# Kernel tuning notes

Measured on AMD Instinct MI355X. Metric: run time of the kernel, lower is better.

## Reference

```python
import jax, jax.numpy as jnp
import numpy as np

N_PROT = 100_000; E_PROT = 1_600_000
N_LIG = 5_000;    E_LIG = 80_000
B_PROT = 64; B_LIG = 1
SEQ = 130; D = 45; K = 4; DIN = 74
PROT_DIMS = [DIN, 50, 45, 45]
LIG_DIMS  = [DIN, 50, 45, 45, 45]
HEAD = [SEQ * D, 2000, 1000, 500, 1]


def setup_inputs() -> dict:
    key = jax.random.key(0)
    ks = iter(jax.random.split(key, 64))
    def rn(shape, scale=1.0):
        return jax.random.normal(next(ks), shape, jnp.float32) * scale
    inp = {
        "prot_x": rn((N_PROT, DIN)),
        "lig_x": rn((N_LIG, DIN)),
    }
    for pref, dims in (("prot", PROT_DIMS), ("lig", LIG_DIMS)):
        for i in range(len(dims) - 1):
            fan_in = (K + 1) * dims[i]
            inp[f"{pref}_W{i}"] = rn((fan_in, dims[i + 1]), fan_in ** -0.5)
            inp[f"{pref}_b{i}"] = jnp.zeros((dims[i + 1],), jnp.float32)
    inp["qkv_w"] = rn((D, 3 * D), D ** -0.5)
    inp["qkv_b"] = jnp.zeros((3 * D,), jnp.float32)
    inp["proj_w"] = rn((D, D), D ** -0.5)
    inp["proj_b"] = jnp.zeros((D,), jnp.float32)
    for i in range(3):
        inp[f"h{i}_w"] = rn((HEAD[i], HEAD[i + 1]), HEAD[i] ** -0.5)
        inp[f"h{i}_b"] = jnp.zeros((HEAD[i + 1],), jnp.float32)
    inp["fc_w"] = rn((HEAD[3], HEAD[4]), HEAD[3] ** -0.5)
    inp["fc_b"] = jnp.zeros((HEAD[4],), jnp.float32)
    inp["prot_src"] = jax.random.randint(next(ks), (E_PROT,), 0, N_PROT, jnp.int32)
    inp["prot_dst"] = jax.random.randint(next(ks), (E_PROT,), 0, N_PROT, jnp.int32)
    # deterministic contiguous subgraph ids guarantee all 64 pockets are non-empty
    inp["prot_gid"] = (jnp.arange(N_PROT) * B_PROT // N_PROT).astype(jnp.int32)
    inp["lig_src"] = jax.random.randint(next(ks), (E_LIG,), 0, N_LIG, jnp.int32)
    inp["lig_dst"] = jax.random.randint(next(ks), (E_LIG,), 0, N_LIG, jnp.int32)
    inp["lig_gid"] = jnp.zeros((N_LIG,), jnp.int32)
    inp["training"] = 0
    return inp


def _tagconv(x, src, dst, W, b, n):
    # DGL TAGConv: h_{k+1} = D^{-1/2} A D^{-1/2} h_k ; out = [h_0..h_K] @ W + b
    deg = jax.ops.segment_sum(jnp.ones_like(dst, x.dtype), dst, num_segments=n)
    norm = jnp.where(deg > 0, deg, 1.0) ** -0.5  # clamp(min=1)^-0.5
    hops = [x]
    h = x
    for _ in range(K):
        h = norm[:, None] * jax.ops.segment_sum((h * norm[:, None])[src], dst, num_segments=n)
        hops.append(h)
    return jnp.concatenate(hops, axis=-1) @ W + b


def _l2norm(x):
    # F.normalize(dim=1): x / max(||x||_2, eps)
    return x / jnp.maximum(jnp.linalg.norm(x, axis=1, keepdims=True), 1e-12)


def _gnn(x, src, dst, gid, Ws, bs, n, ngraphs):
    for W, b in zip(Ws, bs):
        x = _l2norm(jax.nn.relu(_tagconv(x, src, dst, W, b, n)))
        # dropout is identity in eval mode
    return jax.ops.segment_max(x, gid, num_segments=ngraphs)  # DGL MaxPooling


def reference(prot_x, lig_x,
              prot_W0, prot_b0, prot_W1, prot_b1, prot_W2, prot_b2,
              lig_W0, lig_b0, lig_W1, lig_b1, lig_W2, lig_b2, lig_W3, lig_b3,
              qkv_w, qkv_b, proj_w, proj_b,
              h0_w, h0_b, h1_w, h1_b, h2_w, h2_b, fc_w, fc_b,
              prot_src, prot_dst, prot_gid, lig_src, lig_dst, lig_gid, training):
    prot_rep = _gnn(prot_x, prot_src, prot_dst, prot_gid,
                    [prot_W0, prot_W1, prot_W2], [prot_b0, prot_b1, prot_b2],
                    N_PROT, B_PROT)                    # [B_PROT, 45]
    lig_rep = _gnn(lig_x, lig_src, lig_dst, lig_gid,
                   [lig_W0, lig_W1, lig_W2, lig_W3], [lig_b0, lig_b1, lig_b2, lig_b3],
                   N_LIG, B_LIG)                       # [B_LIG, 45]
    n_seq = B_LIG + B_PROT
    seq = jnp.concatenate([lig_rep, prot_rep], axis=0)  # [n_seq, 45]
    seq = jnp.pad(seq, ((0, SEQ - n_seq), (0, 0)))[None]  # [1, 130, 45]

    # eye-based mask exactly as the torch code builds it
    idx = jnp.arange(SEQ)
    valid = idx < n_seq
    mask = jnp.eye(SEQ, dtype=jnp.float32) * (valid[:, None] & valid[None, :])
    mask = mask.at[:, n_seq - 1].set(1.0)
    mask = mask.at[n_seq - 1, :].set(1.0)
    mask = mask.at[n_seq - 1, n_seq - 1].set(0.0)

    qkv = seq @ qkv_w + qkv_b                 # [1, 130, 135]
    q, k, v = jnp.split(qkv, 3, axis=-1)      # single head, head_dim = 45
    attn = jnp.einsum("bqd,bkd->bqk", q, k) * (D ** -0.5)
    attn = jnp.where(mask[None] == 0, -1e9, attn)
    attn = jax.nn.softmax(attn, axis=-1)
    out = jnp.einsum("bqk,bkd->bqd", attn, v) @ proj_w + proj_b  # [1,130,45]

    out = out.reshape(1, SEQ * D)             # [1, 5850]
    for w, b in ((h0_w, h0_b), (h1_w, h1_b), (h2_w, h2_b)):
        out = jax.nn.relu(out @ w + b)        # head dropout off in eval
    return jax.nn.sigmoid(out @ fc_w + fc_b)  # [1, 1]
```

## Files before the change

kernel.cpp:

```cpp
#include <hip/hip_runtime.h>
#include <hip/hip_fp16.h>
#include <cstddef>
#include <cstdint>

namespace {

typedef _Float16 h2v __attribute__((ext_vector_type(2)));

constexpr int NPROT = 100000;
constexpr int EPROT = 1600000;
constexpr int NLIG  = 5000;
constexpr int ELIG  = 80000;


__global__ void hist_kernel(const int* __restrict__ dst, int* __restrict__ cnt, int e) {
  int i = blockIdx.x * 256 + threadIdx.x;
  if (i < e) atomicAdd(&cnt[dst[i]], 1);
}

__global__ void scan1_kernel(const int* __restrict__ cnt, int* __restrict__ rp,
                             int* __restrict__ bsum, float* __restrict__ nrm, int n) {
  __shared__ int wsum[4];
  int t = threadIdx.x;
  int base = blockIdx.x * 1024 + t * 4;
  int v0 = 0, v1 = 0, v2 = 0, v3 = 0;
  if (base + 3 < n) {
    int4 val = *(const int4*)(cnt + base);
    v0 = val.x; v1 = val.y; v2 = val.z; v3 = val.w;
  } else if (base < n) {
    v0 = cnt[base];
    if (base + 1 < n) v1 = cnt[base + 1];
    if (base + 2 < n) v2 = cnt[base + 2];
  }
  if (base < n)     nrm[base]     = 1.0f / sqrtf(fmaxf((float)v0, 1.0f));
  if (base + 1 < n) nrm[base + 1] = 1.0f / sqrtf(fmaxf((float)v1, 1.0f));
  if (base + 2 < n) nrm[base + 2] = 1.0f / sqrtf(fmaxf((float)v2, 1.0f));
  if (base + 3 < n) nrm[base + 3] = 1.0f / sqrtf(fmaxf((float)v3, 1.0f));
  int ts = v0 + v1 + v2 + v3;
  int lane = t & 63, wv = t >> 6;
  int incl = ts;
  #pragma unroll
  for (int off = 1; off < 64; off <<= 1) {
    int o = __shfl_up(incl, off, 64);
    if (lane >= off) incl += o;
  }
  if (lane == 63) wsum[wv] = incl;
  __syncthreads();
  int woff = 0;
  #pragma unroll
  for (int i = 0; i < 4; ++i) if (i < wv) woff += wsum[i];
  int excl = woff + incl - ts;
  int o0 = excl, o1 = o0 + v0, o2 = o1 + v1, o3 = o2 + v2;
  if (base + 3 < n) {
    *(int4*)(rp + base) = make_int4(o0, o1, o2, o3);
  } else if (base < n) {
    rp[base] = o0;
    if (base + 1 < n) rp[base + 1] = o1;
    if (base + 2 < n) rp[base + 2] = o2;
  }
  if (t == 255) bsum[blockIdx.x] = woff + incl;
}

__global__ void scan2_kernel(int* __restrict__ bsum, int nb, int* __restrict__ rp_end) {
  __shared__ int s[256];
  int t = threadIdx.x;
  int v = (t < nb) ? bsum[t] : 0;
  s[t] = v;
  __syncthreads();
  int val = v;
  for (int off = 1; off < 256; off <<= 1) {
    int add = (t >= off) ? s[t - off] : 0;
    __syncthreads();
    val += add;
    s[t] = val;
    __syncthreads();
  }
  if (t < nb) bsum[t] = val - v;
  if (t == 255) *rp_end = val;
}

__global__ void scan3_kernel(int* __restrict__ rp, const int* __restrict__ bsum, int n) {
  int i = blockIdx.x * 256 + threadIdx.x;
  if (i < n) rp[i] += bsum[i >> 10];
}


__global__ void gcur_init_kernel(const int* __restrict__ rp, int* __restrict__ gcur, int n) {
  int t = threadIdx.x;
  if (t < 64) gcur[t] = rp[min(t << 11, n)];
}

__global__ void scat1_kernel(const int* __restrict__ src, const int* __restrict__ dst,
                             int* __restrict__ gcur, uint2* __restrict__ ebuf, int e) {
  __shared__ int lh[64], lb[64];
  int t = threadIdx.x;
  if (t < 64) lh[t] = 0;
  __syncthreads();
  int base = blockIdx.x * 4096;
  int d[16], rk[16];
  #pragma unroll
  for (int j = 0; j < 16; ++j) {
    int i = base + j * 256 + t;
    if (i < e) {
      d[j] = dst[i];
      rk[j] = atomicAdd(&lh[min(d[j] >> 11, 63)], 1);
    }
  }
  __syncthreads();
  if (t < 64 && lh[t] > 0) lb[t] = atomicAdd(&gcur[t], lh[t]);
  __syncthreads();
  #pragma unroll
  for (int j = 0; j < 16; ++j) {
    int i = base + j * 256 + t;
    if (i < e)
      ebuf[lb[min(d[j] >> 11, 63)] + rk[j]] = make_uint2((unsigned)src[i], (unsigned)d[j]);
  }
}

__global__ void scat2_kernel(const uint2* __restrict__ ebuf, const int* __restrict__ rp,
                             int* __restrict__ cur, int* __restrict__ col, int e) {
  int i = blockIdx.x * 256 + threadIdx.x;
  if (i < e) {
    uint2 p = ebuf[i];
    int d = (int)p.y;
    int q = rp[d] + atomicAdd(&cur[d], 1);
    col[q] = (int)p.x;
  }
}


__device__ __forceinline__ float2 cvt_h2(uint32_t u) {
  __half2 h = *reinterpret_cast<__half2*>(&u);
  return make_float2(__low2float(h), __high2float(h));
}

__device__ __forceinline__ h2v bit_h2v(uint32_t u) {
  h2v r;
  *reinterpret_cast<uint32_t*>(&r) = u;
  return r;
}

__global__ void gather_all_kernel(const __half* __restrict__ gin, const int* __restrict__ rp,
                                  const int* __restrict__ col, const float* __restrict__ nrm,
                                  __half* __restrict__ gout, int n, int nbn) {
  int pass = blockIdx.x / nbn;
  int bid = blockIdx.x - pass * nbn;
  int lane = threadIdx.x & 63, wv = threadIdx.x >> 6;
  int q = lane >> 4, r = lane & 15;
  int e_slot = r >> 2, f4 = r & 3;
  int v = bid * 16 + wv * 4 + q;
  bool vok = (v < n);
  int beg = 0, deg = 0;
  if (vok) { beg = rp[v]; deg = rp[v + 1] - beg; }
  const __half* gc = gin + (size_t)pass * n * 16;
  __half* go = gout + (size_t)pass * n * 16;
  float a0 = 0.f, a1 = 0.f, a2 = 0.f, a3 = 0.f;
  for (int base = 0; __any(base < deg); base += 16) {
    int ec = (base + r < deg) ? col[beg + base + r] : -1;
    #pragma unroll
    for (int js = 0; js < 16; js += 4) {
      int sl = (q << 4) + js + e_slot;
      int s0 = __shfl(ec, sl, 64);
      int idx = (s0 >= 0) ? s0 : 0;
      float m = (s0 >= 0) ? 1.f : 0.f;
      uint2 u = *(const uint2*)(gc + (size_t)idx * 16 + (f4 << 2));
      float2 p0 = cvt_h2(u.x), p1 = cvt_h2(u.y);
      a0 = fmaf(m, p0.x, a0); a1 = fmaf(m, p0.y, a1);
      a2 = fmaf(m, p1.x, a2); a3 = fmaf(m, p1.y, a3);
    }
  }
  a0 += __shfl_xor(a0, 4, 64);  a1 += __shfl_xor(a1, 4, 64);
  a2 += __shfl_xor(a2, 4, 64);  a3 += __shfl_xor(a3, 4, 64);
  a0 += __shfl_xor(a0, 8, 64);  a1 += __shfl_xor(a1, 8, 64);
  a2 += __shfl_xor(a2, 8, 64);  a3 += __shfl_xor(a3, 8, 64);
  if (vok && e_slot == 0) {
    float nm = nrm[v];
    float nm2 = nm * nm;
    __half2 w0 = __floats2half2_rn(a0 * nm2, a1 * nm2);
    __half2 w1 = __floats2half2_rn(a2 * nm2, a3 * nm2);
    uint2 st;
    st.x = *reinterpret_cast<uint32_t*>(&w0);
    st.y = *reinterpret_cast<uint32_t*>(&w1);
    *(uint2*)(go + ((size_t)v << 4) + (f4 << 2)) = st;
  }
}

template<int DIN>
__global__ void init_g0_kernel(const float* __restrict__ x, const float* __restrict__ nrm,
                               __half* __restrict__ g0, int n) {
  constexpr int PD = (DIN + 15) & ~15;
  int lane = threadIdx.x & 63;
  int v = blockIdx.x * 4 + (threadIdx.x >> 6);
  if (v >= n) return;
  float nm = nrm[v];
  for (int f = lane; f < PD; f += 64) {
    float val = (f < DIN) ? x[(size_t)v * DIN + f] * nm : 0.f;
    g0[(((size_t)(f >> 4) * n + v) << 4) + (f & 15)] = __float2half(val);
  }
}

__global__ void padw2_kernel(const float* __restrict__ W, uint32_t* __restrict__ Wt,
                             int din, int dout, int pd) {
  int kp2 = 5 * pd / 2;
  int total = dout * kp2;
  int i = blockIdx.x * 256 + threadIdx.x;
  if (i >= total) return;
  int j = i / kp2, k2 = i - j * kp2;
  int f0 = k2 * 2, f1 = f0 + 1;
  int hop0 = f0 / pd, rem0 = f0 - hop0 * pd;
  int hop1 = f1 / pd, rem1 = f1 - hop1 * pd;
  float a = (rem0 < din) ? W[(size_t)(hop0 * din + rem0) * dout + j] : 0.f;
  float b = (rem1 < din) ? W[(size_t)(hop1 * din + rem1) * dout + j] : 0.f;
  __half2 h = __floats2half2_rn(a, b);
  Wt[i] = *reinterpret_cast<uint32_t*>(&h);
}

template<int DIN, int DOUT, bool LAST>
__global__ __launch_bounds__(256) void combine_kernel(
    const __half* __restrict__ gbase, const float* __restrict__ nrm,
    const uint32_t* __restrict__ Wt, const float* __restrict__ bias,
    __half* __restrict__ gnext, float* __restrict__ Xout, int n) {
  constexpr int PD  = (DIN + 15) & ~15;
  constexpr int NCH = PD / 16;
  constexpr int KP2 = 5 * PD / 2;
  constexpr int PDN = (DOUT + 15) & ~15;
  constexpr int QO  = ((DOUT + 7) / 8) * 2;
  __shared__ float ssq[4 * 64];
  int lane = threadIdx.x & 63, wv = threadIdx.x >> 6;
  int v = blockIdx.x * 64 + lane;
  bool vok = (v < n);
  int vc = vok ? v : 0;
  const size_t slabh = (size_t)n * 80;
  int cofs = __builtin_amdgcn_readfirstlane(wv) * QO;
  float acc[QO];
  #pragma unroll
  for (int jj = 0; jj < QO; ++jj) acc[jj] = 0.f;
  for (int hop = 0; hop < 5; ++hop) {
    const __half* hrow = gbase + (size_t)hop * slabh + ((size_t)vc << 4);
    #pragma unroll 1
    for (int ch = 0; ch < NCH; ++ch) {
      uint4 u0 = *(const uint4*)hrow;
      uint4 u1 = *(const uint4*)(hrow + 8);
      uint32_t hp[8] = {u0.x, u0.y, u0.z, u0.w, u1.x, u1.y, u1.z, u1.w};
      int kb = hop * (PD / 2) + ch * 8;
      #pragma unroll
      for (int p = 0; p < 8; ++p) {
        h2v hv = bit_h2v(hp[p]);
        #pragma unroll
        for (int jj = 0; jj < QO; ++jj) {
          h2v wv2 = bit_h2v(Wt[(size_t)(cofs + jj) * KP2 + kb + p]);
          acc[jj] = __builtin_amdgcn_fdot2(hv, wv2, acc[jj], false);
        }
      }
      hrow += ((size_t)n << 4);
    }
  }
  float rn = 1.f / nrm[vc];
  float ss = 0.f;
  #pragma unroll
  for (int jj = 0; jj < QO; ++jj) {
    int j = cofs + jj;
    float y = (j < DOUT) ? fmaxf(bias[j] + acc[jj] * rn, 0.f) : 0.f;
    acc[jj] = y;
    ss += y * y;
  }
  ssq[wv * 64 + lane] = ss;
  __syncthreads();
  if (!vok) return;
  float tot = ssq[lane] + ssq[64 + lane] + ssq[128 + lane] + ssq[192 + lane];
  float sc = 1.f / fmaxf(sqrtf(tot), 1e-12f);
  if (LAST) {
    #pragma unroll
    for (int jj = 0; jj < QO; ++jj) {
      int j = cofs + jj;
      if (j < DOUT) Xout[(size_t)v * DOUT + j] = acc[jj] * sc;
    }
  } else {
    float nm = nrm[v];
    #pragma unroll
    for (int jj = 0; jj < QO; jj += 2) {
      int j0 = cofs + jj;
      float a = (j0 < DOUT) ? acc[jj] * sc * nm : 0.f;
      float b = (j0 + 1 < DOUT) ? acc[jj + 1] * sc * nm : 0.f;
      int ch = j0 >> 4, s = j0 & 15;
      *(__half2*)(gnext + (((size_t)ch * n + v) << 4) + s) = __floats2half2_rn(a, b);
    }
    if (wv == 3) {
      #pragma unroll
      for (int j0 = 4 * QO; j0 < PDN; j0 += 2) {
        int ch = j0 >> 4, s = j0 & 15;
        *(__half2*)(gnext + (((size_t)ch * n + v) << 4) + s) = __floats2half2_rn(0.f, 0.f);
      }
    }
  }
}


template<int DIN, int GS, int DOUT>
__global__ void init_gemm_kernel(const float* __restrict__ x, const float* __restrict__ nrm,
                                 const float* __restrict__ W, const float* __restrict__ bias,
                                 __half* __restrict__ gout, float* __restrict__ y, int n) {
  int lane = threadIdx.x & 63;
  int v = blockIdx.x * 4 + (threadIdx.x >> 6);
  if (v >= n) return;
  float nm = nrm[v];
  const float* xr = x + (size_t)v * DIN;
  float hA = (lane < DIN) ? xr[lane] : 0.f;
  float hB = 0.f;
  if constexpr (DIN > 64) { if (lane + 64 < DIN) hB = xr[lane + 64]; }
  __half* go = gout + (size_t)v * GS;
  if (lane < DIN) go[lane] = __float2half(hA * nm);
  if constexpr (DIN > 64) { if (lane + 64 < DIN) go[lane + 64] = __float2half(hB * nm); }
  int cl = (lane < DOUT) ? lane : 0;
  float acc = bias[cl];
  const float* Wk = W + cl;
  #pragma unroll
  for (int f = 0; f < DIN; ++f) {
    float hf = (f < 64) ? __shfl(hA, f, 64) : __shfl(hB, f - 64, 64);
    acc += hf * Wk[(size_t)f * DOUT];
  }
  if (lane < DOUT) y[(size_t)v * DOUT + lane] = acc;
}

template<int DIN, int GS, int DOUT, bool WRITEG, bool FINAL>
__global__ void fused_hop_kernel(const __half* __restrict__ gin, const int* __restrict__ rp,
                                 const int* __restrict__ col, const float* __restrict__ nrm,
                                 const float* __restrict__ W, __half* __restrict__ gout,
                                 float* __restrict__ y, float* __restrict__ Xout,
                                 int k, int n) {
  int lane = threadIdx.x & 63;
  int v = blockIdx.x * 4 + (threadIdx.x >> 6);
  if (v >= n) return;
  int beg = rp[v], end = rp[v + 1];
  float a0 = 0.f, a1 = 0.f;
  for (int base = beg; base < end; base += 64) {
    int m = end - base; if (m > 64) m = 64;
    int myc = (lane < m) ? col[base + lane] : 0;
    int j = 0;
    for (; j + 8 <= m; j += 8) {
      int ss[8];
      float t0[8], t1[8];
      #pragma unroll
      for (int u = 0; u < 8; ++u) ss[u] = __shfl(myc, j + u, 64);
      #pragma unroll
      for (int u = 0; u < 8; ++u) {
        const __half* rr = gin + (size_t)ss[u] * GS;
        t0[u] = (lane < DIN) ? __half2float(rr[lane]) : 0.f;
        if constexpr (DIN > 64) t1[u] = (lane + 64 < DIN) ? __half2float(rr[lane + 64]) : 0.f;
      }
      #pragma unroll
      for (int u = 0; u < 8; ++u) {
        a0 += t0[u];
        if constexpr (DIN > 64) a1 += t1[u];
      }
    }
    for (; j < m; ++j) {
      int s = __shfl(myc, j, 64);
      const __half* rr = gin + (size_t)s * GS;
      if (lane < DIN) a0 += __half2float(rr[lane]);
      if constexpr (DIN > 64) { if (lane + 64 < DIN) a1 += __half2float(rr[lane + 64]); }
    }
  }
  float nm = nrm[v];
  float hA = a0 * nm, hB = a1 * nm;
  if (WRITEG) {
    __half* go = gout + (size_t)v * GS;
    if (lane < DIN) go[lane] = __float2half(hA * nm);
    if constexpr (DIN > 64) { if (lane + 64 < DIN) go[lane + 64] = __float2half(hB * nm); }
  }
  int cl = (lane < DOUT) ? lane : 0;
  float acc = 0.f;
  if (lane < DOUT) acc = y[(size_t)v * DOUT + lane];
  const float* Wk = W + (size_t)k * DIN * DOUT + cl;
  #pragma unroll
  for (int f = 0; f < DIN; ++f) {
    float hf = (f < 64) ? __shfl(hA, f, 64) : __shfl(hB, f - 64, 64);
    acc += hf * Wk[(size_t)f * DOUT];
  }
  if constexpr (FINAL) {
    float val = (lane < DOUT) ? fmaxf(acc, 0.f) : 0.f;
    float ss2 = val * val;
    #pragma unroll
    for (int off2 = 32; off2 > 0; off2 >>= 1) ss2 += __shfl_xor(ss2, off2, 64);
    float scale = 1.f / fmaxf(sqrtf(ss2), 1e-12f);
    if (lane < DOUT) Xout[(size_t)v * DOUT + lane] = val * scale;
  } else {
    if (lane < DOUT) y[(size_t)v * DOUT + lane] = acc;
  }
}

__global__ void segmax_kernel(const float* __restrict__ X, const int* __restrict__ gid,
                              float* __restrict__ rep, int n, int row_off) {
  __shared__ float tab[4][45];
  __shared__ int gids[256];
  int t = threadIdx.x;
  for (int i = t; i < 4 * 45; i += 256) ((float*)tab)[i] = 0.f;
  int v0 = blockIdx.x * 256;
  int vend = v0 + 256; if (vend > n) vend = n;
  int nv = vend - v0;
  if (t < nv) gids[t] = gid[v0 + t];
  __syncthreads();
  int g0 = gids[0];
  int total = nv * 45;
  for (int i = t; i < total; i += 256) {
    int vl = i / 45, j = i - vl * 45;
    float val = X[(size_t)(v0 + vl) * 45 + j];
    int rel = gids[vl] - g0;
    if (rel >= 0 && rel < 4)
      atomicMax((unsigned int*)&tab[rel][j], __float_as_uint(val));
    else
      atomicMax((unsigned int*)&rep[(size_t)(row_off + gids[vl]) * 45 + j], __float_as_uint(val));
  }
  __syncthreads();
  for (int i = t; i < 4 * 45; i += 256) {
    float val = ((float*)tab)[i];
    if (val > 0.f) {
      int rel = i / 45, j = i - rel * 45;
      atomicMax((unsigned int*)&rep[(size_t)(row_off + g0 + rel) * 45 + j], __float_as_uint(val));
    }
  }
}


__global__ void qkv_kernel(const float* __restrict__ rep, const float* __restrict__ w,
                           const float* __restrict__ b, float* __restrict__ qkv) {
  int i = blockIdx.x;
  int t = threadIdx.x;
  __shared__ float sr[45];
  if (t < 45) sr[t] = (i < 65) ? rep[(size_t)i * 45 + t] : 0.f;
  __syncthreads();
  if (t < 135) {
    float acc = b[t];
    #pragma unroll 5
    for (int d = 0; d < 45; ++d) acc += sr[d] * w[d * 135 + t];
    qkv[(size_t)i * 135 + t] = acc;
  }
}

__global__ void attn_kernel(const float* __restrict__ qkv, const float* __restrict__ proj_w,
                            const float* __restrict__ proj_b, float* __restrict__ ctx) {
  int i = blockIdx.x;
  int t = threadIdx.x;
  __shared__ float q[45];
  __shared__ float p[130];
  __shared__ float red[256];
  __shared__ float ao[45];
  if (t < 45) q[t] = qkv[(size_t)i * 135 + t];
  __syncthreads();
  float s = -1e30f;
  if (t < 130) {
    int j = t;
    float dot = 0.f;
    #pragma unroll 5
    for (int d = 0; d < 45; ++d) dot += q[d] * qkv[(size_t)j * 135 + 45 + d];
    dot *= 0.14907119849998599f;
    bool mz;
    if (i == 64 && j == 64) mz = true;
    else if (i == 64 || j == 64) mz = false;
    else mz = !(i == j && i < 65);
    s = mz ? -1e9f : dot;
  }
  red[t] = s;
  __syncthreads();
  #pragma unroll
  for (int off = 128; off > 0; off >>= 1) {
    if (t < off) red[t] = fmaxf(red[t], red[t + off]);
    __syncthreads();
  }
  float mx = red[0];
  __syncthreads();
  float e = (t < 130) ? expf(s - mx) : 0.f;
  red[t] = e;
  __syncthreads();
  #pragma unroll
  for (int off = 128; off > 0; off >>= 1) {
    if (t < off) red[t] += red[t + off];
    __syncthreads();
  }
  float denom = red[0];
  __syncthreads();
  if (t < 130) p[t] = e / denom;
  __syncthreads();
  if (t < 45) {
    float acc = 0.f;
    for (int j = 0; j < 130; ++j) acc += p[j] * qkv[(size_t)j * 135 + 90 + t];
    ao[t] = acc;
  }
  __syncthreads();
  if (t < 45) {
    float pr = proj_b[t];
    #pragma unroll 5
    for (int e2 = 0; e2 < 45; ++e2) pr += ao[e2] * proj_w[e2 * 45 + t];
    ctx[(size_t)i * 45 + t] = pr;
  }
}


__global__ void bias_init_kernel(const float* __restrict__ b, float* __restrict__ out, int n) {
  int i = blockIdx.x * 256 + threadIdx.x;
  if (i < n) out[i] = b[i];
}

template<bool RELU_IN>
__global__ void fc_splitk_kernel(const float* __restrict__ x, const float* __restrict__ W,
                                 float* __restrict__ out, int nin, int nout, int kchunk) {
  __shared__ float xs[128];
  int k0 = blockIdx.y * kchunk;
  int k1 = k0 + kchunk; if (k1 > nin) k1 = nin;
  int len = k1 - k0;
  for (int i = threadIdx.x; i < len; i += blockDim.x) {
    float v = x[k0 + i];
    xs[i] = RELU_IN ? fmaxf(v, 0.f) : v;
  }
  __syncthreads();
  int j = blockIdx.x * blockDim.x + threadIdx.x;
  if (j < nout) {
    float acc = 0.f;
    const float* Wp = W + (size_t)k0 * nout + j;
    for (int i = 0; i < len; ++i) acc += xs[i] * Wp[(size_t)i * nout];
    atomicAdd(&out[j], acc);
  }
}

__global__ void final_fc_kernel(const float* __restrict__ x, const float* __restrict__ W,
                                const float* __restrict__ b, float* __restrict__ out) {
  __shared__ float red[512];
  int t = threadIdx.x;
  float acc = 0.f;
  if (t < 500) acc = fmaxf(x[t], 0.f) * W[t];
  red[t] = acc;
  __syncthreads();
  #pragma unroll
  for (int off = 256; off > 0; off >>= 1) {
    if (t < off) red[t] += red[t + off];
    __syncthreads();
  }
  if (t == 0) {
    float z = red[0] + b[0];
    out[0] = 1.f / (1.f + expf(-z));
  }
}


struct Bufs {
  __half* slabs;
  __half *ligA, *ligB;
  float *X, *Y, *nrm;
  uint32_t* Wt;
  int *cnt, *cur, *rp, *col, *bsum, *gcur;
  uint2* ebuf;
};

template<int DIN, int DOUT, bool LAST>
void run_layer_prot(const Bufs& g, const float* W, const float* b, int n, hipStream_t st) {
  constexpr int PD = (DIN + 15) & ~15;
  constexpr int NPASS = PD / 16;
  int nbn = (n + 15) / 16;
  size_t slabh = (size_t)n * 80;
  for (int k = 1; k <= 4; ++k)
    gather_all_kernel<<<NPASS * nbn, 256, 0, st>>>(g.slabs + (size_t)(k - 1) * slabh,
                                                   g.rp, g.col, g.nrm,
                                                   g.slabs + (size_t)k * slabh, n, nbn);
  int wtotal = DOUT * (5 * PD / 2);
  padw2_kernel<<<(wtotal + 255) / 256, 256, 0, st>>>(W, g.Wt, DIN, DOUT, PD);
  combine_kernel<DIN, DOUT, LAST><<<(n + 63) / 64, 256, 0, st>>>(
      g.slabs, g.nrm, g.Wt, b, g.slabs, g.X, n);
}

template<int DIN, int GS, int DOUT>
void run_layer_lig(const float* xin, const Bufs& g, const float* W, const float* b,
                   int n, hipStream_t st) {
  int nb = (n + 3) / 4;
  init_gemm_kernel<DIN, GS, DOUT><<<nb, 256, 0, st>>>(xin, g.nrm, W, b, g.ligA, g.Y, n);
  const __half* gin = g.ligA;
  __half* gout = g.ligB;
  for (int k = 1; k <= 4; ++k) {
    if (k < 4)
      fused_hop_kernel<DIN, GS, DOUT, true, false><<<nb, 256, 0, st>>>(gin, g.rp, g.col, g.nrm, W, gout, g.Y, g.X, k, n);
    else
      fused_hop_kernel<DIN, GS, DOUT, false, true><<<nb, 256, 0, st>>>(gin, g.rp, g.col, g.nrm, W, gout, g.Y, g.X, 4, n);
    __half* t = (__half*)gin; gin = gout; gout = t;
  }
}

void build_csr(const int* src, const int* dst, const Bufs& g, int n, int e, hipStream_t st) {
  hipMemsetAsync(g.cnt, 0, (size_t)n * 4, st);
  hipMemsetAsync(g.cur, 0, (size_t)n * 4, st);
  hist_kernel<<<(e + 255) / 256, 256, 0, st>>>(dst, g.cnt, e);
  int nb1 = (n + 1023) / 1024;
  scan1_kernel<<<nb1, 256, 0, st>>>(g.cnt, g.rp, g.bsum, g.nrm, n);
  scan2_kernel<<<1, 256, 0, st>>>(g.bsum, nb1, g.rp + n);
  scan3_kernel<<<(n + 255) / 256, 256, 0, st>>>(g.rp, g.bsum, n);
  gcur_init_kernel<<<1, 64, 0, st>>>(g.rp, g.gcur, n);
  scat1_kernel<<<(e + 4095) / 4096, 256, 0, st>>>(src, dst, g.gcur, g.ebuf, e);
  scat2_kernel<<<(e + 255) / 256, 256, 0, st>>>(g.ebuf, g.rp, g.cur, g.col, e);
}

}

extern "C" void kernel_launch(void* const* d_in, const int* in_sizes, int n_in,
                              void* d_out, int out_size, void* d_ws, size_t ws_size,
                              hipStream_t stream) {
  (void)in_sizes; (void)n_in; (void)out_size;

  const float* prot_x = (const float*)d_in[0];
  const float* lig_x  = (const float*)d_in[1];
  const float* pW[3] = {(const float*)d_in[2], (const float*)d_in[4], (const float*)d_in[6]};
  const float* pB[3] = {(const float*)d_in[3], (const float*)d_in[5], (const float*)d_in[7]};
  const float* lW[4] = {(const float*)d_in[8], (const float*)d_in[10], (const float*)d_in[12], (const float*)d_in[14]};
  const float* lB[4] = {(const float*)d_in[9], (const float*)d_in[11], (const float*)d_in[13], (const float*)d_in[15]};
  const float* qkv_w = (const float*)d_in[16];
  const float* qkv_b = (const float*)d_in[17];
  const float* proj_w = (const float*)d_in[18];
  const float* proj_b = (const float*)d_in[19];
  const float* h0_w = (const float*)d_in[20];
  const float* h0_b = (const float*)d_in[21];
  const float* h1_w = (const float*)d_in[22];
  const float* h1_b = (const float*)d_in[23];
  const float* h2_w = (const float*)d_in[24];
  const float* h2_b = (const float*)d_in[25];
  const float* fc_w = (const float*)d_in[26];
  const float* fc_b = (const float*)d_in[27];
  const int* prot_src = (const int*)d_in[28];
  const int* prot_dst = (const int*)d_in[29];
  const int* prot_gid = (const int*)d_in[30];
  const int* lig_src  = (const int*)d_in[31];
  const int* lig_dst  = (const int*)d_in[32];
  const int* lig_gid  = (const int*)d_in[33];

  char* w = (char*)d_ws;
  size_t off = 0;
  auto alloc = [&](size_t bytes) -> void* {
    void* p = w + off;
    off += (bytes + 255) & ~(size_t)255;
    return p;
  };
  __half* slabs = (__half*)alloc((size_t)5 * NPROT * 80 * 2);
  __half* ligA  = (__half*)alloc((size_t)NLIG * 96 * 2);
  __half* ligB  = (__half*)alloc((size_t)NLIG * 96 * 2);
  float* X   = (float*)alloc((size_t)NPROT * 45 * 4);
  float* Y   = (float*)alloc((size_t)NLIG * 50 * 4);
  float* nrm = (float*)alloc((size_t)NPROT * 4);
  uint32_t* Wt = (uint32_t*)alloc((size_t)50 * 200 * 4 + 256);
  int* cnt   = (int*)alloc((size_t)NPROT * 4);
  int* cur   = (int*)alloc((size_t)NPROT * 4);
  int* rp    = (int*)alloc(((size_t)NPROT + 1) * 4);
  int* colb  = (int*)alloc((size_t)EPROT * 4);
  int* bsum  = (int*)alloc((size_t)256 * 4);
  int* gcur  = (int*)alloc((size_t)64 * 4);
  float* rep = (float*)alloc((size_t)65 * 45 * 4);
  float* qkvb = (float*)alloc((size_t)130 * 135 * 4);
  float* ctx  = (float*)alloc((size_t)5850 * 4);
  float* hb0  = (float*)alloc((size_t)2000 * 4);
  float* hb1  = (float*)alloc((size_t)1000 * 4);
  float* hb2  = (float*)alloc((size_t)500 * 4);
  if (off > ws_size) return;

  hipMemsetAsync(rep, 0, (size_t)65 * 45 * 4, stream);

  Bufs g{slabs, ligA, ligB, X, Y, nrm, Wt, cnt, cur, rp, colb, bsum, gcur,
         (uint2*)slabs };

  build_csr(prot_src, prot_dst, g, NPROT, EPROT, stream);
  init_g0_kernel<74><<<(NPROT + 3) / 4, 256, 0, stream>>>(prot_x, g.nrm, g.slabs, NPROT);
  run_layer_prot<74, 50, false>(g, pW[0], pB[0], NPROT, stream);
  run_layer_prot<50, 45, false>(g, pW[1], pB[1], NPROT, stream);
  run_layer_prot<45, 45, true >(g, pW[2], pB[2], NPROT, stream);
  segmax_kernel<<<(NPROT + 255) / 256, 256, 0, stream>>>(g.X, prot_gid, rep, NPROT, 1);

  build_csr(lig_src, lig_dst, g, NLIG, ELIG, stream);
  run_layer_lig<74, 96, 50>(lig_x, g, lW[0], lB[0], NLIG, stream);
  run_layer_lig<50, 64, 45>(g.X, g, lW[1], lB[1], NLIG, stream);
  run_layer_lig<45, 64, 45>(g.X, g, lW[2], lB[2], NLIG, stream);
  run_layer_lig<45, 64, 45>(g.X, g, lW[3], lB[3], NLIG, stream);
  segmax_kernel<<<(NLIG + 255) / 256, 256, 0, stream>>>(g.X, lig_gid, rep, NLIG, 0);

  qkv_kernel<<<130, 256, 0, stream>>>(rep, qkv_w, qkv_b, qkvb);
  attn_kernel<<<130, 256, 0, stream>>>(qkvb, proj_w, proj_b, ctx);

  bias_init_kernel<<<8, 256, 0, stream>>>(h0_b, hb0, 2000);
  fc_splitk_kernel<false><<<dim3(8, 64), 256, 0, stream>>>(ctx, h0_w, hb0, 5850, 2000, 92);
  bias_init_kernel<<<4, 256, 0, stream>>>(h1_b, hb1, 1000);
  fc_splitk_kernel<true><<<dim3(4, 32), 256, 0, stream>>>(hb0, h1_w, hb1, 2000, 1000, 63);
  bias_init_kernel<<<2, 256, 0, stream>>>(h2_b, hb2, 500);
  fc_splitk_kernel<true><<<dim3(2, 16), 256, 0, stream>>>(hb1, h2_w, hb2, 1000, 500, 63);
  final_fc_kernel<<<1, 512, 0, stream>>>(hb2, fc_w, fc_b, (float*)d_out);
}
```

Baseline: 1.243 ms.

## Pad CSR rows to multiples of 16 with a zero sentinel row to drop gather masking

Each node's CSR segment is padded to a multiple of 16 entries. Padding slots point at an extra all-zero feature row (index n) appended to every slab, so the gather loop needs no bounds mask or multiply and can issue four independent loads per iteration. This requires larger column and slab buffers, a fill kernel over the column array, and new kernels that zero the sentinel rows. Group cursors now come from per-block counts instead of rp. The cost is extra memory traffic: average degree is 16, so padding adds roughly 8 dummy edges per node, all hitting one row that stays in cache.

```diff
diff --git a/kernel.cpp b/kernel.cpp
--- a/kernel.cpp
+++ b/kernel.cpp
@@ -36,7 +36,9 @@
   if (base + 1 < n) nrm[base + 1] = 1.0f / sqrtf(fmaxf((float)v1, 1.0f));
   if (base + 2 < n) nrm[base + 2] = 1.0f / sqrtf(fmaxf((float)v2, 1.0f));
   if (base + 3 < n) nrm[base + 3] = 1.0f / sqrtf(fmaxf((float)v3, 1.0f));
-  int ts = v0 + v1 + v2 + v3;
+  int p0 = (v0 + 15) & ~15, p1 = (v1 + 15) & ~15;
+  int p2 = (v2 + 15) & ~15, p3 = (v3 + 15) & ~15;
+  int ts = p0 + p1 + p2 + p3;
   int lane = t & 63, wv = t >> 6;
   int incl = ts;
   #pragma unroll
@@ -50,7 +52,7 @@
   #pragma unroll
   for (int i = 0; i < 4; ++i) if (i < wv) woff += wsum[i];
   int excl = woff + incl - ts;
-  int o0 = excl, o1 = o0 + v0, o2 = o1 + v1, o3 = o2 + v2;
+  int o0 = excl, o1 = o0 + p0, o2 = o1 + p1, o3 = o2 + p2;
   if (base + 3 < n) {
     *(int4*)(rp + base) = make_int4(o0, o1, o2, o3);
   } else if (base < n) {
@@ -84,10 +86,43 @@
   if (i < n) rp[i] += bsum[i >> 10];
 }
 
-
-__global__ void gcur_init_kernel(const int* __restrict__ rp, int* __restrict__ gcur, int n) {
-  int t = threadIdx.x;
-  if (t < 64) gcur[t] = rp[min(t << 11, n)];
+__global__ void fill_kernel(int* __restrict__ p, int val, int cnt) {
+  int i = blockIdx.x * 256 + threadIdx.x;
+  if (i < cnt) p[i] = val;
+}
+
+__global__ void bcnt_kernel(const int* __restrict__ cnt, int* __restrict__ bcnt, int n) {
+  __shared__ int red[256];
+  int b = blockIdx.x;
+  int t = threadIdx.x;
+  int s = 0;
+  int beg = b << 11, end = min(beg + 2048, n);
+  for (int i = beg + t; i < end; i += 256) s += cnt[i];
+  red[t] = s;
+  __syncthreads();
+  #pragma unroll
+  for (int off = 128; off > 0; off >>= 1) {
+    if (t < off) red[t] += red[t + off];
+    __syncthreads();
+  }
+  if (t == 0) bcnt[b] = red[0];
+}
+
+__global__ void gcur_init_kernel(const int* __restrict__ bcnt, int* __restrict__ gcur) {
+  __shared__ int s[64];
+  int t = threadIdx.x;
+  int v = bcnt[t];
+  s[t] = v;
+  __syncthreads();
+  int val = v;
+  for (int off = 1; off < 64; off <<= 1) {
+    int add = (t >= off) ? s[t - off] : 0;
+    __syncthreads();
+    val += add;
+    s[t] = val;
+    __syncthreads();
+  }
+  gcur[t] = val - v;
 }
 
 __global__ void scat1_kernel(const int* __restrict__ src, const int* __restrict__ dst,
@@ -138,6 +173,24 @@
   h2v r;
   *reinterpret_cast<uint32_t*>(&r) = u;
   return r;
+}
+
+__global__ void zrow_prot_kernel(__half* __restrict__ slabs, int n) {
+  int i = threadIdx.x;
+  if (i < 400) {
+    int slab = i / 80, rem = i - slab * 80;
+    int c = rem >> 4, s = rem & 15;
+    size_t slabh = (size_t)(n + 1) * 80;
+    slabs[(size_t)slab * slabh + (((size_t)c * (n + 1) + n) << 4) + s] = __float2half(0.f);
+  }
+}
+
+__global__ void zrow_lig_kernel(__half* __restrict__ ligA, __half* __restrict__ ligB, int n) {
+  int i = threadIdx.x;
+  if (i < 96) {
+    ligA[(size_t)n * 96 + i] = __float2half(0.f);
+    ligB[(size_t)n * 96 + i] = __float2half(0.f);
+  }
 }
 
 __global__ void gather_all_kernel(const __half* __restrict__ gin, const int* __restrict__ rp,
@@ -150,24 +203,32 @@
   int e_slot = r >> 2, f4 = r & 3;
   int v = bid * 16 + wv * 4 + q;
   bool vok = (v < n);
-  int beg = 0, deg = 0;
-  if (vok) { beg = rp[v]; deg = rp[v + 1] - beg; }
-  const __half* gc = gin + (size_t)pass * n * 16;
-  __half* go = gout + (size_t)pass * n * 16;
+  int beg = 0, pdeg = 0;
+  if (vok) { beg = rp[v]; pdeg = rp[v + 1] - beg; }
+  size_t cbase = (size_t)pass * (n + 1) * 16;
+  const __half* gc = gin + cbase;
+  __half* go = gout + cbase;
+  int sl = (q << 4) + e_slot;
   float a0 = 0.f, a1 = 0.f, a2 = 0.f, a3 = 0.f;
-  for (int base = 0; __any(base < deg); base += 16) {
-    int ec = (base + r < deg) ? col[beg + base + r] : -1;
-    #pragma unroll
-    for (int js = 0; js < 16; js += 4) {
-      int sl = (q << 4) + js + e_slot;
-      int s0 = __shfl(ec, sl, 64);
-      int idx = (s0 >= 0) ? s0 : 0;
-      float m = (s0 >= 0) ? 1.f : 0.f;
-      uint2 u = *(const uint2*)(gc + (size_t)idx * 16 + (f4 << 2));
-      float2 p0 = cvt_h2(u.x), p1 = cvt_h2(u.y);
-      a0 = fmaf(m, p0.x, a0); a1 = fmaf(m, p0.y, a1);
-      a2 = fmaf(m, p1.x, a2); a3 = fmaf(m, p1.y, a3);
-    }
+  for (int base = 0; __any(base < pdeg); base += 16) {
+    int ec = (base + r < pdeg) ? col[beg + base + r] : n;
+    int s0 = __shfl(ec, sl, 64);
+    int s1 = __shfl(ec, sl + 4, 64);
+    int s2 = __shfl(ec, sl + 8, 64);
+    int s3 = __shfl(ec, sl + 12, 64);
+    uint2 u0 = *(const uint2*)(gc + ((size_t)s0 << 4) + (f4 << 2));
+    uint2 u1 = *(const uint2*)(gc + ((size_t)s1 << 4) + (f4 << 2));
+    uint2 u2 = *(const uint2*)(gc + ((size_t)s2 << 4) + (f4 << 2));
+    uint2 u3 = *(const uint2*)(gc + ((size_t)s3 << 4) + (f4 << 2));
+    float2 p;
+    p = cvt_h2(u0.x); a0 += p.x; a1 += p.y;
+    p = cvt_h2(u0.y); a2 += p.x; a3 += p.y;
+    p = cvt_h2(u1.x); a0 += p.x; a1 += p.y;
+    p = cvt_h2(u1.y); a2 += p.x; a3 += p.y;
+    p = cvt_h2(u2.x); a0 += p.x; a1 += p.y;
+    p = cvt_h2(u2.y); a2 += p.x; a3 += p.y;
+    p = cvt_h2(u3.x); a0 += p.x; a1 += p.y;
+    p = cvt_h2(u3.y); a2 += p.x; a3 += p.y;
   }
   a0 += __shfl_xor(a0, 4, 64);  a1 += __shfl_xor(a1, 4, 64);
   a2 += __shfl_xor(a2, 4, 64);  a3 += __shfl_xor(a3, 4, 64);
@@ -195,7 +256,7 @@
   float nm = nrm[v];
   for (int f = lane; f < PD; f += 64) {
     float val = (f < DIN) ? x[(size_t)v * DIN + f] * nm : 0.f;
-    g0[(((size_t)(f >> 4) * n + v) << 4) + (f & 15)] = __float2half(val);
+    g0[(((size_t)(f >> 4) * (n + 1) + v) << 4) + (f & 15)] = __float2half(val);
   }
 }
 
@@ -230,7 +291,8 @@
   int v = blockIdx.x * 64 + lane;
   bool vok = (v < n);
   int vc = vok ? v : 0;
-  const size_t slabh = (size_t)n * 80;
+  const size_t slabh = (size_t)(n + 1) * 80;
+  const size_t chstep = ((size_t)(n + 1) << 4);
   int cofs = __builtin_amdgcn_readfirstlane(wv) * QO;
   float acc[QO];
   #pragma unroll
@@ -252,7 +314,7 @@
           acc[jj] = __builtin_amdgcn_fdot2(hv, wv2, acc[jj], false);
         }
       }
-      hrow += ((size_t)n << 4);
+      hrow += chstep;
     }
   }
   float rn = 1.f / nrm[vc];
@@ -283,13 +345,13 @@
       float a = (j0 < DOUT) ? acc[jj] * sc * nm : 0.f;
       float b = (j0 + 1 < DOUT) ? acc[jj + 1] * sc * nm : 0.f;
       int ch = j0 >> 4, s = j0 & 15;
-      *(__half2*)(gnext + (((size_t)ch * n + v) << 4) + s) = __floats2half2_rn(a, b);
+      *(__half2*)(gnext + (((size_t)ch * (n + 1) + v) << 4) + s) = __floats2half2_rn(a, b);
     }
     if (wv == 3) {
       #pragma unroll
       for (int j0 = 4 * QO; j0 < PDN; j0 += 2) {
         int ch = j0 >> 4, s = j0 & 15;
-        *(__half2*)(gnext + (((size_t)ch * n + v) << 4) + s) = __floats2half2_rn(0.f, 0.f);
+        *(__half2*)(gnext + (((size_t)ch * (n + 1) + v) << 4) + s) = __floats2half2_rn(0.f, 0.f);
       }
     }
   }
@@ -547,7 +609,7 @@
   __half *ligA, *ligB;
   float *X, *Y, *nrm;
   uint32_t* Wt;
-  int *cnt, *cur, *rp, *col, *bsum, *gcur;
+  int *cnt, *cur, *rp, *col, *bsum, *gcur, *bcnt;
   uint2* ebuf;
 };
 
@@ -556,7 +618,7 @@
   constexpr int PD = (DIN + 15) & ~15;
   constexpr int NPASS = PD / 16;
   int nbn = (n + 15) / 16;
-  size_t slabh = (size_t)n * 80;
+  size_t slabh = (size_t)(n + 1) * 80;
   for (int k = 1; k <= 4; ++k)
     gather_all_kernel<<<NPASS * nbn, 256, 0, st>>>(g.slabs + (size_t)(k - 1) * slabh,
                                                    g.rp, g.col, g.nrm,
@@ -567,23 +629,24 @@
       g.slabs, g.nrm, g.Wt, b, g.slabs, g.X, n);
 }
 
-template<int DIN, int GS, int DOUT>
+template<int DIN, int DOUT>
 void run_layer_lig(const float* xin, const Bufs& g, const float* W, const float* b,
                    int n, hipStream_t st) {
   int nb = (n + 3) / 4;
-  init_gemm_kernel<DIN, GS, DOUT><<<nb, 256, 0, st>>>(xin, g.nrm, W, b, g.ligA, g.Y, n);
+  init_gemm_kernel<DIN, 96, DOUT><<<nb, 256, 0, st>>>(xin, g.nrm, W, b, g.ligA, g.Y, n);
   const __half* gin = g.ligA;
   __half* gout = g.ligB;
   for (int k = 1; k <= 4; ++k) {
     if (k < 4)
-      fused_hop_kernel<DIN, GS, DOUT, true, false><<<nb, 256, 0, st>>>(gin, g.rp, g.col, g.nrm, W, gout, g.Y, g.X, k, n);
+      fused_hop_kernel<DIN, 96, DOUT, true, false><<<nb, 256, 0, st>>>(gin, g.rp, g.col, g.nrm, W, gout, g.Y, g.X, k, n);
     else
-      fused_hop_kernel<DIN, GS, DOUT, false, true><<<nb, 256, 0, st>>>(gin, g.rp, g.col, g.nrm, W, gout, g.Y, g.X, 4, n);
+      fused_hop_kernel<DIN, 96, DOUT, false, true><<<nb, 256, 0, st>>>(gin, g.rp, g.col, g.nrm, W, gout, g.Y, g.X, 4, n);
     __half* t = (__half*)gin; gin = gout; gout = t;
   }
 }
 
-void build_csr(const int* src, const int* dst, const Bufs& g, int n, int e, hipStream_t st) {
+void build_csr(const int* src, const int* dst, const Bufs& g, int n, int e,
+               int colcap, hipStream_t st) {
   hipMemsetAsync(g.cnt, 0, (size_t)n * 4, st);
   hipMemsetAsync(g.cur, 0, (size_t)n * 4, st);
   hist_kernel<<<(e + 255) / 256, 256, 0, st>>>(dst, g.cnt, e);
@@ -591,7 +654,9 @@
   scan1_kernel<<<nb1, 256, 0, st>>>(g.cnt, g.rp, g.bsum, g.nrm, n);
   scan2_kernel<<<1, 256, 0, st>>>(g.bsum, nb1, g.rp + n);
   scan3_kernel<<<(n + 255) / 256, 256, 0, st>>>(g.rp, g.bsum, n);
-  gcur_init_kernel<<<1, 64, 0, st>>>(g.rp, g.gcur, n);
+  fill_kernel<<<(colcap + 255) / 256, 256, 0, st>>>(g.col, n, colcap);
+  bcnt_kernel<<<64, 256, 0, st>>>(g.cnt, g.bcnt, n);
+  gcur_init_kernel<<<1, 64, 0, st>>>(g.bcnt, g.gcur);
   scat1_kernel<<<(e + 4095) / 4096, 256, 0, st>>>(src, dst, g.gcur, g.ebuf, e);
   scat2_kernel<<<(e + 255) / 256, 256, 0, st>>>(g.ebuf, g.rp, g.cur, g.col, e);
 }
@@ -635,9 +700,10 @@
     off += (bytes + 255) & ~(size_t)255;
     return p;
   };
-  __half* slabs = (__half*)alloc((size_t)5 * NPROT * 80 * 2);
-  __half* ligA  = (__half*)alloc((size_t)NLIG * 96 * 2);
-  __half* ligB  = (__half*)alloc((size_t)NLIG * 96 * 2);
+  constexpr int COLCAP = EPROT + 16 * NPROT;
+  __half* slabs = (__half*)alloc((size_t)5 * (NPROT + 1) * 80 * 2);
+  __half* ligA  = (__half*)alloc(((size_t)NLIG * 96 + 96) * 2);
+  __half* ligB  = (__half*)alloc(((size_t)NLIG * 96 + 96) * 2);
   float* X   = (float*)alloc((size_t)NPROT * 45 * 4);
   float* Y   = (float*)alloc((size_t)NLIG * 50 * 4);
   float* nrm = (float*)alloc((size_t)NPROT * 4);
@@ -645,9 +711,10 @@
   int* cnt   = (int*)alloc((size_t)NPROT * 4);
   int* cur   = (int*)alloc((size_t)NPROT * 4);
   int* rp    = (int*)alloc(((size_t)NPROT + 1) * 4);
-  int* colb  = (int*)alloc((size_t)EPROT * 4);
+  int* colb  = (int*)alloc((size_t)COLCAP * 4);
   int* bsum  = (int*)alloc((size_t)256 * 4);
   int* gcur  = (int*)alloc((size_t)64 * 4);
+  int* bcntb = (int*)alloc((size_t)64 * 4);
   float* rep = (float*)alloc((size_t)65 * 45 * 4);
   float* qkvb = (float*)alloc((size_t)130 * 135 * 4);
   float* ctx  = (float*)alloc((size_t)5850 * 4);
@@ -658,21 +725,23 @@
 
   hipMemsetAsync(rep, 0, (size_t)65 * 45 * 4, stream);
 
-  Bufs g{slabs, ligA, ligB, X, Y, nrm, Wt, cnt, cur, rp, colb, bsum, gcur,
+  Bufs g{slabs, ligA, ligB, X, Y, nrm, Wt, cnt, cur, rp, colb, bsum, gcur, bcntb,
          (uint2*)slabs };
 
-  build_csr(prot_src, prot_dst, g, NPROT, EPROT, stream);
+  build_csr(prot_src, prot_dst, g, NPROT, EPROT, COLCAP, stream);
+  zrow_prot_kernel<<<1, 512, 0, stream>>>(g.slabs, NPROT);
   init_g0_kernel<74><<<(NPROT + 3) / 4, 256, 0, stream>>>(prot_x, g.nrm, g.slabs, NPROT);
   run_layer_prot<74, 50, false>(g, pW[0], pB[0], NPROT, stream);
   run_layer_prot<50, 45, false>(g, pW[1], pB[1], NPROT, stream);
   run_layer_prot<45, 45, true >(g, pW[2], pB[2], NPROT, stream);
   segmax_kernel<<<(NPROT + 255) / 256, 256, 0, stream>>>(g.X, prot_gid, rep, NPROT, 1);
 
-  build_csr(lig_src, lig_dst, g, NLIG, ELIG, stream);
-  run_layer_lig<74, 96, 50>(lig_x, g, lW[0], lB[0], NLIG, stream);
-  run_layer_lig<50, 64, 45>(g.X, g, lW[1], lB[1], NLIG, stream);
-  run_layer_lig<45, 64, 45>(g.X, g, lW[2], lB[2], NLIG, stream);
-  run_layer_lig<45, 64, 45>(g.X, g, lW[3], lB[3], NLIG, stream);
+  build_csr(lig_src, lig_dst, g, NLIG, ELIG, ELIG + 16 * NLIG, stream);
+  zrow_lig_kernel<<<1, 128, 0, stream>>>(g.ligA, g.ligB, NLIG);
+  run_layer_lig<74, 50>(lig_x, g, lW[0], lB[0], NLIG, stream);
+  run_layer_lig<50, 45>(g.X, g, lW[1], lB[1], NLIG, stream);
+  run_layer_lig<45, 45>(g.X, g, lW[2], lB[2], NLIG, stream);
+  run_layer_lig<45, 45>(g.X, g, lW[3], lB[3], NLIG, stream);
   segmax_kernel<<<(NLIG + 255) / 256, 256, 0, stream>>>(g.X, lig_gid, rep, NLIG, 0);
 
   qkv_kernel<<<130, 256, 0, stream>>>(rep, qkv_w, qkv_b, qkvb);
```

Result: slower. 1.307 ms (+5.1%).
